# Performance work log

Hardware: AMD Instinct MI355X
Metric: run time of the kernel (lower is better)

The kernel has to match this reference:

```python
import jax, jax.numpy as jnp
import numpy as np

EPS = 1e-5
K = 20

def _leaky(x):
    return jnp.where(x >= 0, x, 0.2 * x)

def _bn(y, g, b, axes):
    mean = jnp.mean(y, axis=axes, keepdims=True)
    var = jnp.var(y, axis=axes, keepdims=True)
    shp = [1] * y.ndim
    shp[1] = -1
    return g.reshape(shp) * (y - mean) * jax.lax.rsqrt(var + EPS) + b.reshape(shp)

def _edge_conv(x, w, g, b, k):
    # x: [B, C, N]; w: [F, 2C]
    xt = jnp.swapaxes(x, 1, 2)  # [B, N, C]
    sq = jnp.sum(xt * xt, axis=-1)  # [B, N]
    # pairwise_distance[b,i,j] = -||x_i - x_j||^2
    d = 2.0 * jnp.einsum('bnc,bmc->bnm', xt, xt) - sq[:, :, None] - sq[:, None, :]
    idx = jax.lax.top_k(d, k)[1]  # [B, N, k] nearest neighbors (self included)
    feat = jax.vmap(lambda f, i: f[i])(xt, idx)  # [B, N, k, C]
    center = xt[:, :, None, :]
    h = jnp.concatenate([feat - center, jnp.broadcast_to(center, feat.shape)], axis=-1)  # [B,N,k,2C]
    y = jnp.einsum('bnkc,fc->bfnk', h, w)  # 1x1 Conv2d, no bias
    y = _leaky(_bn(y, g, b, axes=(0, 2, 3)))
    return jnp.max(y, axis=-1)  # max over neighbors -> [B, F, N]

def setup_inputs() -> dict:
    key = jax.random.key(0)
    ks = jax.random.split(key, 16)
    B, N, C0 = 8, 2048, 3
    dims = [64, 64, 128, 256]
    out_dim = 1024
    inp = {"x": jax.random.normal(ks[0], (B, N, C0), dtype=jnp.float32)}
    cin = C0
    for i, f in enumerate(dims):
        inp[f"w{i}"] = jax.random.normal(ks[1 + i], (f, 2 * cin), dtype=jnp.float32) * (1.0 / np.sqrt(2 * cin))
        inp[f"g{i}"] = jnp.ones((f,), dtype=jnp.float32)
        inp[f"b{i}"] = jnp.zeros((f,), dtype=jnp.float32)
        cin = f
    tot = sum(dims)
    inp["wf"] = jax.random.normal(ks[10], (out_dim, tot), dtype=jnp.float32) * (1.0 / np.sqrt(tot))
    inp["gf"] = jnp.ones((out_dim,), dtype=jnp.float32)
    inp["bf"] = jnp.zeros((out_dim,), dtype=jnp.float32)
    return inp

def reference(x, w0, g0, b0, w1, g1, b1, w2, g2, b2, w3, g3, b3, wf, gf, bf):
    h = jnp.swapaxes(x, 1, 2)  # [B, C, N]
    feats = []
    for (w, g, b) in ((w0, g0, b0), (w1, g1, b1), (w2, g2, b2), (w3, g3, b3)):
        h = _edge_conv(h, w, g, b, K)
        feats.append(h)
    cat = jnp.concatenate(feats, axis=1)  # [B, sum(dims), N]
    y = jnp.einsum('bcn,fc->bfn', cat, wf)  # 1x1 Conv1d, no bias
    y = _leaky(_bn(y, gf, bf, axes=(0, 2)))
    return jnp.swapaxes(y, 1, 2)  # [B, N, out_dim]
```

## Files before the change

kernel.cpp:

```cpp
#include <hip/hip_runtime.h>

#define NPTS 2048
#define BATCH 8
#define KNN 20

__global__ void k_sqnorm(const float* __restrict__ fin, int stride, int off,
                         float* __restrict__ sq, int C) {
  int i = blockIdx.x * 256 + threadIdx.x;
  const float* r = fin + (size_t)i * stride + off;
  float a = 0.f;
  for (int c = 0; c < C; ++c) a = fmaf(r[c], r[c], a);
  sq[i] = a;
}

__global__ void __launch_bounds__(256) k_screen(const float* __restrict__ fin,
                                                int stride, int off, int KK,
                                                const float* __restrict__ sq,
                                                int b, float* __restrict__ D) {
  __shared__ float As[16][68];
  __shared__ float Bs[16][68];
  int tid = threadIdx.x;
  int n0 = blockIdx.y * 64, m0 = blockIdx.x * 64;
  const float* fb = fin + (size_t)b * NPTS * stride + off;
  int lr = tid >> 2;
  int lk = (tid & 3) * 4;
  float acc[4][4];
  #pragma unroll
  for (int i = 0; i < 4; ++i)
    #pragma unroll
    for (int j = 0; j < 4; ++j) acc[i][j] = 0.f;
  for (int k0 = 0; k0 < KK; k0 += 16) {
    float4 av, bv;
    const float* arow = fb + (size_t)(n0 + lr) * stride + k0 + lk;
    const float* brow = fb + (size_t)(m0 + lr) * stride + k0 + lk;
    int rem = KK - k0;
    if (lk + 4 <= rem) { av = *(const float4*)arow; bv = *(const float4*)brow; }
    else {
      av.x = (lk + 0 < rem) ? arow[0] : 0.f;  bv.x = (lk + 0 < rem) ? brow[0] : 0.f;
      av.y = (lk + 1 < rem) ? arow[1] : 0.f;  bv.y = (lk + 1 < rem) ? brow[1] : 0.f;
      av.z = (lk + 2 < rem) ? arow[2] : 0.f;  bv.z = (lk + 2 < rem) ? brow[2] : 0.f;
      av.w = (lk + 3 < rem) ? arow[3] : 0.f;  bv.w = (lk + 3 < rem) ? brow[3] : 0.f;
    }
    __syncthreads();
    As[lk+0][lr] = av.x; As[lk+1][lr] = av.y; As[lk+2][lr] = av.z; As[lk+3][lr] = av.w;
    Bs[lk+0][lr] = bv.x; Bs[lk+1][lr] = bv.y; Bs[lk+2][lr] = bv.z; Bs[lk+3][lr] = bv.w;
    __syncthreads();
    int ty = tid >> 4, tx = tid & 15;
    #pragma unroll
    for (int kk = 0; kk < 16; ++kk) {
      float4 a = *(const float4*)&As[kk][ty * 4];
      float4 b2 = *(const float4*)&Bs[kk][tx * 4];
      acc[0][0] = fmaf(a.x, b2.x, acc[0][0]); acc[0][1] = fmaf(a.x, b2.y, acc[0][1]);
      acc[0][2] = fmaf(a.x, b2.z, acc[0][2]); acc[0][3] = fmaf(a.x, b2.w, acc[0][3]);
      acc[1][0] = fmaf(a.y, b2.x, acc[1][0]); acc[1][1] = fmaf(a.y, b2.y, acc[1][1]);
      acc[1][2] = fmaf(a.y, b2.z, acc[1][2]); acc[1][3] = fmaf(a.y, b2.w, acc[1][3]);
      acc[2][0] = fmaf(a.z, b2.x, acc[2][0]); acc[2][1] = fmaf(a.z, b2.y, acc[2][1]);
      acc[2][2] = fmaf(a.z, b2.z, acc[2][2]); acc[2][3] = fmaf(a.z, b2.w, acc[2][3]);
      acc[3][0] = fmaf(a.w, b2.x, acc[3][0]); acc[3][1] = fmaf(a.w, b2.y, acc[3][1]);
      acc[3][2] = fmaf(a.w, b2.z, acc[3][2]); acc[3][3] = fmaf(a.w, b2.w, acc[3][3]);
    }
  }
  int ty = tid >> 4, tx = tid & 15;
  const float* sqb = sq + b * NPTS;
  #pragma unroll
  for (int i = 0; i < 4; ++i) {
    float sn = sqb[n0 + ty * 4 + i];
    #pragma unroll
    for (int j = 0; j < 4; ++j) {
      float sm = sqb[m0 + tx * 4 + j];
      D[(size_t)(n0 + ty * 4 + i) * NPTS + m0 + tx * 4 + j] = 2.f * acc[i][j] - sn - sm;
    }
  }
}

__device__ inline unsigned f2u(float f) {
  unsigned b = __float_as_uint(f);
  return b ^ (unsigned)(((int)b >> 31) | 0x80000000);
}

__device__ inline void row_select(const float (&dv)[32], int wt,
                                  unsigned* __restrict__ hist,
                                  unsigned* __restrict__ cntp,
                                  int*      __restrict__ candc,
                                  double*   __restrict__ candd,
                                  const float* __restrict__ ctrrow,
                                  const float* __restrict__ finb,
                                  int stride, int off, int C,
                                  int* __restrict__ outp) {
  unsigned u[32];
  #pragma unroll
  for (int s = 0; s < 32; ++s) u[s] = f2u(dv[s]);

  unsigned K = 32;
  unsigned pbits = 0;
  unsigned maskhi = 0;
  for (int lvl = 0; lvl < 3; ++lvl) {
    int sh = 24 - 8 * lvl;
    #pragma unroll
    for (int j = 0; j < 4; ++j) hist[wt * 4 + j] = 0u;
    __threadfence_block();
    #pragma unroll
    for (int s = 0; s < 32; ++s) {
      unsigned uu = u[s];
      if ((uu & maskhi) == pbits) atomicAdd(&hist[(uu >> sh) & 255u], 1u);
    }
    __threadfence_block();
    unsigned h[4];
    #pragma unroll
    for (int j = 0; j < 4; ++j) h[j] = hist[wt * 4 + j];
    unsigned lsum = h[0] + h[1] + h[2] + h[3];
    unsigned acc = lsum;
    #pragma unroll
    for (int o = 1; o < 64; o <<= 1) {
      unsigned t = __shfl_down(acc, o, 64);
      acc += (wt + o < 64) ? t : 0u;
    }
    unsigned S = acc - lsum;
    unsigned ca3 = S;
    unsigned ca2 = ca3 + h[3];
    unsigned ca1 = ca2 + h[2];
    unsigned ca0 = ca1 + h[1];
    unsigned ca[4] = {ca0, ca1, ca2, ca3};
    int myb = -1; unsigned myK = 0;
    #pragma unroll
    for (int j = 3; j >= 0; --j)
      if (myb < 0 && ca[j] < K && K <= ca[j] + h[j]) { myb = 4 * wt + j; myK = K - ca[j]; }
    unsigned long long mk = __ballot(myb >= 0);
    int src = __ffsll((unsigned long long)mk) - 1;
    int B = __shfl(myb, src, 64);
    K = (unsigned)__shfl((int)myK, src, 64);
    pbits |= ((unsigned)B & 255u) << sh;
    maskhi |= 255u << sh;
  }
  unsigned T = pbits;

  if (wt == 0) *cntp = 0u;
  __threadfence_block();
  #pragma unroll
  for (int s = 0; s < 32; ++s) {
    if (u[s] >= T) {
      unsigned pos = atomicAdd(cntp, 1u);
      if (pos < 64u) candc[pos] = ((s >> 2) << 8) + (wt << 2) + (s & 3);
    }
  }
  __threadfence_block();
  int cnt = (int)min(*cntp, 64u);

  int m; double dd;
  if (wt < cnt) {
    m = candc[wt];
    dd = 0.0;
    const float* nr = finb + (size_t)m * stride + off;
    int C4 = C & ~3;
    for (int c = 0; c < C4; c += 4) {
      float4 xv = *(const float4*)(nr + c);
      double d0 = (double)ctrrow[c + 0] - (double)xv.x;
      dd = fma(d0, d0, dd);
      double d1 = (double)ctrrow[c + 1] - (double)xv.y;
      dd = fma(d1, d1, dd);
      double d2 = (double)ctrrow[c + 2] - (double)xv.z;
      dd = fma(d2, d2, dd);
      double d3 = (double)ctrrow[c + 3] - (double)xv.w;
      dd = fma(d3, d3, dd);
    }
    for (int c = C4; c < C; ++c) {
      double df = (double)ctrrow[c] - (double)nr[c];
      dd = fma(df, df, dd);
    }
  } else { dd = 1e300; m = 1 << 30; }
  candd[wt] = dd;
  __threadfence_block();

  int rank = 0;
  for (int j = 0; j < cnt; ++j) {
    double dj = candd[j]; int mj = candc[j];
    rank += (dj < dd || (dj == dd && mj < m)) ? 1 : 0;
  }
  if (wt < cnt && rank < KNN) outp[rank] = m;
}

__global__ void __launch_bounds__(256) k_select(const float* __restrict__ D,
                                                const float* __restrict__ fin,
                                                int stride, int off, int C, int b,
                                                int* __restrict__ idxo) {
  __shared__ unsigned histS[4][256];
  __shared__ unsigned cntS[4];
  __shared__ int candcS[4][64];
  __shared__ double canddS[4][64];
  int tid = threadIdx.x;
  int wave = tid >> 6, wt = tid & 63;
  int n = blockIdx.x * 4 + wave;
  float dv[32];
  const float4* rp = (const float4*)(D + (size_t)n * NPTS) + wt;
  #pragma unroll
  for (int j = 0; j < 8; ++j) {
    float4 v = rp[64 * j];
    dv[j*4+0] = v.x; dv[j*4+1] = v.y; dv[j*4+2] = v.z; dv[j*4+3] = v.w;
  }
  const float* finb = fin + (size_t)b * NPTS * stride;
  row_select(dv, wt, histS[wave], &cntS[wave], candcS[wave], canddS[wave],
             finb + (size_t)n * stride + off, finb, stride, off, C,
             idxo + ((size_t)b * NPTS + n) * KNN);
}


__global__ void k_wprep(const float* __restrict__ w, float* __restrict__ wc,
                        int C, int F) {
  int i = blockIdx.x * 256 + threadIdx.x;
  if (i >= 2 * F * C) return;
  int n = i / C, c = i - n * C;
  wc[i] = (n < F) ? w[(size_t)n * 2 * C + c]
                  : w[(size_t)(n - F) * 2 * C + C + c] - w[(size_t)(n - F) * 2 * C + c];
}

template <int C>
__global__ void __launch_bounds__(256) k_zgemm(const float* __restrict__ A, int lda, int off,
                                               const float* __restrict__ WC, int W2F,
                                               float* __restrict__ ZT) {
  __shared__ float As[C][68];
  __shared__ float Ws[C][68];
  int tid = threadIdx.x;
  int m0 = blockIdx.y * 64, f0 = blockIdx.x * 64;
  for (int i = tid; i < 64 * C; i += 256) {
    int r = i / C, c = i - r * C;
    As[c][r] = A[(size_t)(m0 + r) * lda + off + c];
    Ws[c][r] = WC[(size_t)(f0 + r) * C + c];
  }
  __syncthreads();
  int ty = tid >> 4, tx = tid & 15;
  float acc[4][4];
  #pragma unroll
  for (int i = 0; i < 4; ++i)
    #pragma unroll
    for (int j = 0; j < 4; ++j) acc[i][j] = 0.f;
  for (int kk = 0; kk < C; ++kk) {
    float4 a = *(const float4*)&As[kk][ty * 4];
    float4 b = *(const float4*)&Ws[kk][tx * 4];
    acc[0][0] = fmaf(a.x, b.x, acc[0][0]); acc[0][1] = fmaf(a.x, b.y, acc[0][1]);
    acc[0][2] = fmaf(a.x, b.z, acc[0][2]); acc[0][3] = fmaf(a.x, b.w, acc[0][3]);
    acc[1][0] = fmaf(a.y, b.x, acc[1][0]); acc[1][1] = fmaf(a.y, b.y, acc[1][1]);
    acc[1][2] = fmaf(a.y, b.z, acc[1][2]); acc[1][3] = fmaf(a.y, b.w, acc[1][3]);
    acc[2][0] = fmaf(a.z, b.x, acc[2][0]); acc[2][1] = fmaf(a.z, b.y, acc[2][1]);
    acc[2][2] = fmaf(a.z, b.z, acc[2][2]); acc[2][3] = fmaf(a.z, b.w, acc[2][3]);
    acc[3][0] = fmaf(a.w, b.x, acc[3][0]); acc[3][1] = fmaf(a.w, b.y, acc[3][1]);
    acc[3][2] = fmaf(a.w, b.z, acc[3][2]); acc[3][3] = fmaf(a.w, b.w, acc[3][3]);
  }
  #pragma unroll
  for (int i = 0; i < 4; ++i)
    #pragma unroll
    for (int j = 0; j < 4; ++j)
      ZT[(size_t)(m0 + ty * 4 + i) * W2F + f0 + tx * 4 + j] = acc[i][j];
}

template <int F, int PL, int SP>
__global__ void __launch_bounds__(256) k_gather(const float* __restrict__ ZT, int W2F,
                                                const int* __restrict__ idxb,
                                                const float* __restrict__ g,
                                                float* __restrict__ cat, int catoff,
                                                double* __restrict__ stats) {
  int tid = threadIdx.x;
  int pl = tid / F, f = tid & (F - 1);
  float gg = g[f];
  double s = 0.0, ss = 0.0;
  int nbase = blockIdx.x * (PL * SP) + pl * SP;
  for (int sp = 0; sp < SP; ++sp) {
    int n = nbase + sp;
    int gbase = n & ~(NPTS - 1);
    const int* ip = idxb + n * KNN;
    float T = ZT[(size_t)n * W2F + F + f];
    float mx = -1e30f, mn = 1e30f;
    #pragma unroll
    for (int k = 0; k < KNN; ++k) {
      int m = ip[k];
      float z = ZT[(size_t)(gbase + m) * W2F + f];
      float y = z + T;
      mx = fmaxf(mx, y); mn = fminf(mn, y);
      double yd = (double)y;
      s += yd; ss = fma(yd, yd, ss);
    }
    cat[(size_t)n * 512 + catoff + f] = (gg >= 0.f) ? mx : mn;
  }
  atomicAdd(&stats[f], s);
  atomicAdd(&stats[F + f], ss);
}

__global__ void k_bn(float* __restrict__ cat, const double* __restrict__ stats,
                     const float* __restrict__ g, const float* __restrict__ bb,
                     int Fbits, int catoff) {
  int i = blockIdx.x * 256 + threadIdx.x;
  int F = 1 << Fbits;
  int f = i & (F - 1);
  int bn = i >> Fbits;
  const double invCnt = 1.0 / (double)(BATCH * NPTS * KNN);
  double mean = stats[f] * invCnt;
  double ex2  = stats[F + f] * invCnt;
  double var  = ex2 - mean * mean;
  if (var < 0.0) var = 0.0;
  double rs   = rsqrt(var + 1e-5);
  float* p = &cat[(size_t)bn * 512 + catoff + f];
  float y = *p;
  float t = (float)((double)g[f] * ((double)y - mean) * rs + (double)bb[f]);
  *p = (t >= 0.f) ? t : 0.2f * t;
}

__global__ void __launch_bounds__(256) k_gemm(const float* __restrict__ A,
                                              const float* __restrict__ Bw,
                                              float* __restrict__ Cc) {
  __shared__ float As[16][68];
  __shared__ float Bs[16][68];
  int tid = threadIdx.x;
  int m0 = blockIdx.y * 64, f0 = blockIdx.x * 64;
  int ty = tid >> 4, tx = tid & 15;
  int lr = tid >> 2;
  int lk = (tid & 3) * 4;
  float acc[4][4];
  #pragma unroll
  for (int i = 0; i < 4; ++i)
    #pragma unroll
    for (int j = 0; j < 4; ++j) acc[i][j] = 0.f;
  for (int k0 = 0; k0 < 512; k0 += 16) {
    float4 av = *(const float4*)&A [(size_t)(m0 + lr) * 512 + k0 + lk];
    float4 bv = *(const float4*)&Bw[(size_t)(f0 + lr) * 512 + k0 + lk];
    __syncthreads();
    As[lk+0][lr] = av.x; As[lk+1][lr] = av.y; As[lk+2][lr] = av.z; As[lk+3][lr] = av.w;
    Bs[lk+0][lr] = bv.x; Bs[lk+1][lr] = bv.y; Bs[lk+2][lr] = bv.z; Bs[lk+3][lr] = bv.w;
    __syncthreads();
    #pragma unroll
    for (int kk = 0; kk < 16; ++kk) {
      float4 a = *(const float4*)&As[kk][ty * 4];
      float4 b = *(const float4*)&Bs[kk][tx * 4];
      acc[0][0] = fmaf(a.x, b.x, acc[0][0]); acc[0][1] = fmaf(a.x, b.y, acc[0][1]);
      acc[0][2] = fmaf(a.x, b.z, acc[0][2]); acc[0][3] = fmaf(a.x, b.w, acc[0][3]);
      acc[1][0] = fmaf(a.y, b.x, acc[1][0]); acc[1][1] = fmaf(a.y, b.y, acc[1][1]);
      acc[1][2] = fmaf(a.y, b.z, acc[1][2]); acc[1][3] = fmaf(a.y, b.w, acc[1][3]);
      acc[2][0] = fmaf(a.z, b.x, acc[2][0]); acc[2][1] = fmaf(a.z, b.y, acc[2][1]);
      acc[2][2] = fmaf(a.z, b.z, acc[2][2]); acc[2][3] = fmaf(a.z, b.w, acc[2][3]);
      acc[3][0] = fmaf(a.w, b.x, acc[3][0]); acc[3][1] = fmaf(a.w, b.y, acc[3][1]);
      acc[3][2] = fmaf(a.w, b.z, acc[3][2]); acc[3][3] = fmaf(a.w, b.w, acc[3][3]);
    }
  }
  #pragma unroll
  for (int i = 0; i < 4; ++i)
    #pragma unroll
    for (int j = 0; j < 4; ++j)
      Cc[(size_t)(m0 + ty * 4 + i) * 1024 + f0 + tx * 4 + j] = acc[i][j];
}

__global__ void k_fstats(const float* __restrict__ y, double* __restrict__ st) {
  int tid = threadIdx.x;
  int r0 = blockIdx.x * 256;
  double s[4] = {0,0,0,0}, ss[4] = {0,0,0,0};
  for (int r = r0; r < r0 + 256; ++r) {
    const float* row = y + (size_t)r * 1024;
    #pragma unroll
    for (int q = 0; q < 4; ++q) {
      double v = (double)row[tid + 256 * q];
      s[q] += v; ss[q] = fma(v, v, ss[q]);
    }
  }
  #pragma unroll
  for (int q = 0; q < 4; ++q) {
    atomicAdd(&st[tid + 256 * q], s[q]);
    atomicAdd(&st[1024 + tid + 256 * q], ss[q]);
  }
}

__global__ void k_fnorm(float* __restrict__ y, const double* __restrict__ st,
                        const float* __restrict__ g, const float* __restrict__ bb) {
  int i = blockIdx.x * 256 + threadIdx.x;
  int f = i & 1023;
  const double invCnt = 1.0 / 16384.0;
  double mean = st[f] * invCnt;
  double ex2  = st[1024 + f] * invCnt;
  double var  = ex2 - mean * mean;
  if (var < 0.0) var = 0.0;
  double rs   = rsqrt(var + 1e-5);
  float v = y[i];
  float t = (float)((double)g[f] * ((double)v - mean) * rs + (double)bb[f]);
  y[i] = (t >= 0.f) ? t : 0.2f * t;
}

extern "C" void kernel_launch(void* const* d_in, const int* in_sizes, int n_in,
                              void* d_out, int out_size, void* d_ws, size_t ws_size,
                              hipStream_t stream) {
  const float* x  = (const float*)d_in[0];
  const float* W[4]  = {(const float*)d_in[1], (const float*)d_in[4],
                        (const float*)d_in[7], (const float*)d_in[10]};
  const float* G[4]  = {(const float*)d_in[2], (const float*)d_in[5],
                        (const float*)d_in[8], (const float*)d_in[11]};
  const float* Bb[4] = {(const float*)d_in[3], (const float*)d_in[6],
                        (const float*)d_in[9], (const float*)d_in[12]};
  const float* wf = (const float*)d_in[13];
  const float* gf = (const float*)d_in[14];
  const float* bf = (const float*)d_in[15];
  float* out = (float*)d_out;

  float* ws  = (float*)d_ws;
  float* SQ  = ws;
  float* CAT = SQ + 16384;
  float* ZT  = CAT + 8388608;
  float* WC  = ZT + 8388608;
  double* ST = (double*)(WC + 65536);
  int*   IDX = (int*)(ST + 2048);

  const int Cs[4]      = {3, 64, 64, 128};
  const int Fs[4]      = {64, 64, 128, 256};
  const int Fbits[4]   = {6, 6, 7, 8};
  const int offs[4]    = {0, 0, 64, 128};
  const int strides[4] = {3, 512, 512, 512};
  const int catoffs[4] = {0, 64, 128, 256};

  for (int l = 0; l < 4; ++l) {
    const float* fin = (l == 0) ? x : CAT;
    int C = Cs[l], F = Fs[l];
    int W2F = 2 * F;
    k_sqnorm<<<dim3(BATCH * NPTS / 256), 256, 0, stream>>>(fin, strides[l], offs[l], SQ, C);
    for (int b = 0; b < BATCH; ++b) {
      k_screen<<<dim3(NPTS / 64, NPTS / 64), 256, 0, stream>>>(fin, strides[l], offs[l], C, SQ, b, ZT);
      k_select<<<dim3(NPTS / 4), 256, 0, stream>>>(ZT, fin, strides[l], offs[l], C, b, IDX);
    }
    k_wprep<<<dim3((2 * F * C + 255) / 256), 256, 0, stream>>>(W[l], WC, C, F);
    switch (C) {
      case 3:   k_zgemm<3>  <<<dim3(W2F / 64, 256), 256, 0, stream>>>(fin, strides[l], offs[l], WC, W2F, ZT); break;
      case 64:  k_zgemm<64> <<<dim3(W2F / 64, 256), 256, 0, stream>>>(fin, strides[l], offs[l], WC, W2F, ZT); break;
      default:  k_zgemm<128><<<dim3(W2F / 64, 256), 256, 0, stream>>>(fin, strides[l], offs[l], WC, W2F, ZT); break;
    }
    (void)hipMemsetAsync(ST, 0, 2 * F * sizeof(double), stream);
    switch (F) {
      case 64:  k_gather<64, 4, 16><<<dim3(16384 / 64), 256, 0, stream>>>(ZT, W2F, IDX, G[l], CAT, catoffs[l], ST); break;
      case 128: k_gather<128, 2, 16><<<dim3(16384 / 32), 256, 0, stream>>>(ZT, W2F, IDX, G[l], CAT, catoffs[l], ST); break;
      default:  k_gather<256, 1, 16><<<dim3(16384 / 16), 256, 0, stream>>>(ZT, W2F, IDX, G[l], CAT, catoffs[l], ST); break;
    }
    k_bn<<<dim3(BATCH * NPTS * F / 256), 256, 0, stream>>>(CAT, ST, G[l], Bb[l], Fbits[l], catoffs[l]);
  }

  k_gemm<<<dim3(1024 / 64, 16384 / 64), 256, 0, stream>>>(CAT, wf, out);
  (void)hipMemsetAsync(ST, 0, 2048 * sizeof(double), stream);
  k_fstats<<<dim3(64), 256, 0, stream>>>(out, ST);
  k_fnorm<<<dim3(16384 * 1024 / 256), 256, 0, stream>>>(out, ST, gf, bf);
}
```

Before: 1.967 ms.

## Batch two clouds per kNN launch and use bitwise threshold search in select

```diff
diff --git a/kernel.cpp b/kernel.cpp
--- a/kernel.cpp
+++ b/kernel.cpp
@@ -16,10 +16,12 @@
 __global__ void __launch_bounds__(256) k_screen(const float* __restrict__ fin,
                                                 int stride, int off, int KK,
                                                 const float* __restrict__ sq,
-                                                int b, float* __restrict__ D) {
+                                                int bbase, float* __restrict__ Dbase) {
   __shared__ float As[16][68];
   __shared__ float Bs[16][68];
   int tid = threadIdx.x;
+  int b = bbase + blockIdx.z;
+  float* D = Dbase + (size_t)blockIdx.z * NPTS * NPTS;
   int n0 = blockIdx.y * 64, m0 = blockIdx.x * 64;
   const float* fb = fin + (size_t)b * NPTS * stride + off;
   int lr = tid >> 2;
@@ -79,10 +81,8 @@
 }
 
 __device__ inline void row_select(const float (&dv)[32], int wt,
-                                  unsigned* __restrict__ hist,
-                                  unsigned* __restrict__ cntp,
-                                  int*      __restrict__ candc,
-                                  double*   __restrict__ candd,
+                                  int*    __restrict__ candc,
+                                  double* __restrict__ candd,
                                   const float* __restrict__ ctrrow,
                                   const float* __restrict__ finb,
                                   int stride, int off, int C,
@@ -91,104 +91,77 @@
   #pragma unroll
   for (int s = 0; s < 32; ++s) u[s] = f2u(dv[s]);
 
-  unsigned K = 32;
-  unsigned pbits = 0;
-  unsigned maskhi = 0;
-  for (int lvl = 0; lvl < 3; ++lvl) {
-    int sh = 24 - 8 * lvl;
-    #pragma unroll
-    for (int j = 0; j < 4; ++j) hist[wt * 4 + j] = 0u;
-    __threadfence_block();
-    #pragma unroll
-    for (int s = 0; s < 32; ++s) {
-      unsigned uu = u[s];
-      if ((uu & maskhi) == pbits) atomicAdd(&hist[(uu >> sh) & 255u], 1u);
-    }
-    __threadfence_block();
-    unsigned h[4];
-    #pragma unroll
-    for (int j = 0; j < 4; ++j) h[j] = hist[wt * 4 + j];
-    unsigned lsum = h[0] + h[1] + h[2] + h[3];
-    unsigned acc = lsum;
-    #pragma unroll
-    for (int o = 1; o < 64; o <<= 1) {
-      unsigned t = __shfl_down(acc, o, 64);
-      acc += (wt + o < 64) ? t : 0u;
-    }
-    unsigned S = acc - lsum;
-    unsigned ca3 = S;
-    unsigned ca2 = ca3 + h[3];
-    unsigned ca1 = ca2 + h[2];
-    unsigned ca0 = ca1 + h[1];
-    unsigned ca[4] = {ca0, ca1, ca2, ca3};
-    int myb = -1; unsigned myK = 0;
-    #pragma unroll
-    for (int j = 3; j >= 0; --j)
-      if (myb < 0 && ca[j] < K && K <= ca[j] + h[j]) { myb = 4 * wt + j; myK = K - ca[j]; }
-    unsigned long long mk = __ballot(myb >= 0);
-    int src = __ffsll((unsigned long long)mk) - 1;
-    int B = __shfl(myb, src, 64);
-    K = (unsigned)__shfl((int)myK, src, 64);
-    pbits |= ((unsigned)B & 255u) << sh;
-    maskhi |= 255u << sh;
-  }
-  unsigned T = pbits;
-
-  if (wt == 0) *cntp = 0u;
+  unsigned P = 0u;
+  for (int k = 31; k >= 8; --k) {
+    unsigned Pt = P | (1u << k);
+    int bc = 0;
+    #pragma unroll
+    for (int s = 0; s < 32; ++s) bc += (u[s] >= Pt) ? 1 : 0;
+    #pragma unroll
+    for (int o = 1; o < 64; o <<= 1) bc += __shfl_xor(bc, o, 64);
+    if (bc >= 32) P = Pt;
+  }
+  const unsigned T = P;
+
+  int cnt = 0;
+  #pragma unroll
+  for (int s = 0; s < 32; ++s) {
+    bool pred = (u[s] >= T);
+    unsigned long long mk = __ballot(pred);
+    if (pred) {
+      int pos = cnt + (int)__popcll(mk & ((1ull << wt) - 1ull));
+      if (pos < 128) candc[pos] = ((s >> 2) << 8) + (wt << 2) + (s & 3);
+    }
+    cnt += (int)__popcll(mk);
+  }
+  if (cnt > 128) cnt = 128;
   __threadfence_block();
-  #pragma unroll
-  for (int s = 0; s < 32; ++s) {
-    if (u[s] >= T) {
-      unsigned pos = atomicAdd(cntp, 1u);
-      if (pos < 64u) candc[pos] = ((s >> 2) << 8) + (wt << 2) + (s & 3);
-    }
+
+  double dq[2]; int mq[2];
+  #pragma unroll
+  for (int q = 0; q < 2; ++q) {
+    int ci = wt + 64 * q;
+    if (ci < cnt) {
+      int m = candc[ci];
+      double dd = 0.0;
+      const float* nr = finb + (size_t)m * stride + off;
+      int C4 = C & ~3;
+      for (int c = 0; c < C4; c += 4) {
+        float4 xv = *(const float4*)(nr + c);
+        double d0 = (double)ctrrow[c + 0] - (double)xv.x; dd = fma(d0, d0, dd);
+        double d1 = (double)ctrrow[c + 1] - (double)xv.y; dd = fma(d1, d1, dd);
+        double d2 = (double)ctrrow[c + 2] - (double)xv.z; dd = fma(d2, d2, dd);
+        double d3 = (double)ctrrow[c + 3] - (double)xv.w; dd = fma(d3, d3, dd);
+      }
+      for (int c = C4; c < C; ++c) {
+        double df = (double)ctrrow[c] - (double)nr[c]; dd = fma(df, df, dd);
+      }
+      dq[q] = dd; mq[q] = m;
+    } else { dq[q] = 1e300; mq[q] = 1 << 30; }
+    candd[ci] = dq[q];
   }
   __threadfence_block();
-  int cnt = (int)min(*cntp, 64u);
-
-  int m; double dd;
-  if (wt < cnt) {
-    m = candc[wt];
-    dd = 0.0;
-    const float* nr = finb + (size_t)m * stride + off;
-    int C4 = C & ~3;
-    for (int c = 0; c < C4; c += 4) {
-      float4 xv = *(const float4*)(nr + c);
-      double d0 = (double)ctrrow[c + 0] - (double)xv.x;
-      dd = fma(d0, d0, dd);
-      double d1 = (double)ctrrow[c + 1] - (double)xv.y;
-      dd = fma(d1, d1, dd);
-      double d2 = (double)ctrrow[c + 2] - (double)xv.z;
-      dd = fma(d2, d2, dd);
-      double d3 = (double)ctrrow[c + 3] - (double)xv.w;
-      dd = fma(d3, d3, dd);
-    }
-    for (int c = C4; c < C; ++c) {
-      double df = (double)ctrrow[c] - (double)nr[c];
-      dd = fma(df, df, dd);
-    }
-  } else { dd = 1e300; m = 1 << 30; }
-  candd[wt] = dd;
-  __threadfence_block();
-
-  int rank = 0;
+
+  int r0 = 0, r1 = 0;
   for (int j = 0; j < cnt; ++j) {
     double dj = candd[j]; int mj = candc[j];
-    rank += (dj < dd || (dj == dd && mj < m)) ? 1 : 0;
-  }
-  if (wt < cnt && rank < KNN) outp[rank] = m;
-}
-
-__global__ void __launch_bounds__(256) k_select(const float* __restrict__ D,
+    r0 += (dj < dq[0] || (dj == dq[0] && mj < mq[0])) ? 1 : 0;
+    r1 += (dj < dq[1] || (dj == dq[1] && mj < mq[1])) ? 1 : 0;
+  }
+  if (wt < cnt && r0 < KNN) outp[r0] = mq[0];
+  if (wt + 64 < cnt && r1 < KNN) outp[r1] = mq[1];
+}
+
+__global__ void __launch_bounds__(256) k_select(const float* __restrict__ Dbase,
                                                 const float* __restrict__ fin,
-                                                int stride, int off, int C, int b,
+                                                int stride, int off, int C, int bbase,
                                                 int* __restrict__ idxo) {
-  __shared__ unsigned histS[4][256];
-  __shared__ unsigned cntS[4];
-  __shared__ int candcS[4][64];
-  __shared__ double canddS[4][64];
+  __shared__ int candcS[4][128];
+  __shared__ double canddS[4][128];
   int tid = threadIdx.x;
   int wave = tid >> 6, wt = tid & 63;
+  int b = bbase + blockIdx.y;
+  const float* D = Dbase + (size_t)blockIdx.y * NPTS * NPTS;
   int n = blockIdx.x * 4 + wave;
   float dv[32];
   const float4* rp = (const float4*)(D + (size_t)n * NPTS) + wt;
@@ -198,7 +171,7 @@
     dv[j*4+0] = v.x; dv[j*4+1] = v.y; dv[j*4+2] = v.z; dv[j*4+3] = v.w;
   }
   const float* finb = fin + (size_t)b * NPTS * stride;
-  row_select(dv, wt, histS[wave], &cntS[wave], candcS[wave], canddS[wave],
+  row_select(dv, wt, candcS[wave], canddS[wave],
              finb + (size_t)n * stride + off, finb, stride, off, C,
              idxo + ((size_t)b * NPTS + n) * KNN);
 }
@@ -415,9 +388,9 @@
     int C = Cs[l], F = Fs[l];
     int W2F = 2 * F;
     k_sqnorm<<<dim3(BATCH * NPTS / 256), 256, 0, stream>>>(fin, strides[l], offs[l], SQ, C);
-    for (int b = 0; b < BATCH; ++b) {
-      k_screen<<<dim3(NPTS / 64, NPTS / 64), 256, 0, stream>>>(fin, strides[l], offs[l], C, SQ, b, ZT);
-      k_select<<<dim3(NPTS / 4), 256, 0, stream>>>(ZT, fin, strides[l], offs[l], C, b, IDX);
+    for (int bb = 0; bb < BATCH; bb += 2) {
+      k_screen<<<dim3(NPTS / 64, NPTS / 64, 2), 256, 0, stream>>>(fin, strides[l], offs[l], C, SQ, bb, ZT);
+      k_select<<<dim3(NPTS / 4, 2), 256, 0, stream>>>(ZT, fin, strides[l], offs[l], C, bb, IDX);
     }
     k_wprep<<<dim3((2 * F * C + 255) / 256), 256, 0, stream>>>(W[l], WC, C, F);
     switch (C) {
```

After: 1.680 ms. -14.6%, faster.
